# Kernel optimization log

Measured on AMD Instinct MI355X. Metric: run time of the kernel, lower is better.

Reference implementation:

```python
import jax, jax.numpy as jnp
import numpy as np
from jax.scipy.special import ndtr, ndtri, logsumexp

M_FREQ = 50
N_LAYERS = 5
MIXTURE = 5
MU = 4.0 * np.pi * 1e-7
LOG_2PI = float(np.log(2.0 * np.pi))
BATCH = 131072
SAMPL = 1


def setup_inputs() -> dict:
    key = jax.random.key(0)
    k1, k2, k3, k4 = jax.random.split(key, 4)
    x = jax.random.uniform(k1, (BATCH, N_LAYERS + 2 * M_FREQ), jnp.float32)
    s = jax.random.normal(k2, (BATCH, MIXTURE, 2 * N_LAYERS + 1), jnp.float32)
    u_cat = jax.random.uniform(k3, (SAMPL, BATCH), jnp.float32)
    u_trunc = jax.random.uniform(k4, (SAMPL, BATCH, N_LAYERS), jnp.float32)
    return {"x": x, "s": s, "u_cat": u_cat, "u_trunc": u_trunc}


def _elbo(x, s, u_cat, u_trunc):
    n = N_LAYERS
    B = x.shape[0]
    freqs = jnp.asarray(10.0 ** np.linspace(-2, 3, M_FREQ), jnp.float32)
    # --- mixture-density head ---
    sq = jnp.square(s[:, :, 2 * n])
    pro = sq / jnp.sum(sq, axis=1, keepdims=True)              # [B, M] (fun_part_uni)
    sig = jax.nn.softplus(s[:, :, n:2 * n])                    # [B, M, n]
    loc = 4.0 * jax.nn.sigmoid(s[:, :, :n])                    # [B, M, n]
    # --- sample q = Mixture(TruncatedNormal(loc, sig, 0.1, 3.9)) via inverse CDF ---
    cum = jnp.cumsum(pro, axis=1)                              # [B, M]
    comp = jnp.clip(jnp.sum(u_cat[:, :, None] > cum[None], axis=-1), 0, MIXTURE - 1)  # [S,B] int
    b_idx = jnp.arange(B)[None, :]
    loc_s = loc[b_idx, comp]                                   # [S, B, n]
    sig_s = sig[b_idx, comp]
    a = (0.1 - loc_s) / sig_s
    b = (3.9 - loc_s) / sig_s
    Fa, Fb = ndtr(a), ndtr(b)
    z = ndtri(Fa + u_trunc * (Fb - Fa))
    samples_q = jnp.clip(loc_s + sig_s * z, 0.1, 3.9)          # [S, B, n]
    # --- FP: recursive MT impedance forward model, vectorized over frequencies ---
    thick = x[:, :n]                                            # [B, n]
    res = 10.0 ** samples_q                                     # [S, B, n]
    w = (2.0 * np.pi) * freqs[:, None, None]                    # [m, 1, 1]
    ZR = jnp.sqrt(w * MU * res[:, :, n - 1] / 2.0)              # [m, S, B]
    ZC = ZR
    for j in range(n - 2, -1, -1):
        rj = res[:, :, j]                                       # [S, B]
        th = thick[:, j]                                        # [B]
        dj = jnp.sqrt(w * MU * (1.0 / rj) / 2.0)                # [m, S, B]
        wj = dj * rj                                            # wjR == wjC in source
        t = 2.0 * th * dj
        e = jnp.exp(-t)
        ejR = e * jnp.cos(t)   # cos(-t) == cos(t)
        ejC = -e * jnp.sin(t)
        den = jnp.square(wj + ZR) + jnp.square(wj + ZC)
        rjR = (2.0 * jnp.square(wj) - jnp.square(ZR) - jnp.square(ZC)) / den
        rjC = (2.0 * wj * ZR - 2.0 * wj * ZC) / den
        reR = rjR * ejR - rjC * ejC
        reC = rjR * ejC + rjC * ejR
        den2 = jnp.square(1.0 + reR) + jnp.square(reC)
        auxR = (1.0 - jnp.square(reR) - jnp.square(reC)) / den2
        auxC = -(2.0 * reC) / den2
        ZR, ZC = wj * auxR - wj * auxC, wj * auxC + wj * auxR
    absZ2 = jnp.square(ZR) + jnp.square(ZC)                     # [m, S, B]
    aRes = jnp.log10(absZ2 / (MU * w))
    phas = jnp.arctan2(ZC, ZR)
    S = samples_q.shape[0]
    formation = jnp.transpose(jnp.concatenate([aRes, phas], 0), (2, 1, 0)).reshape(S, B, 2 * M_FREQ)
    # --- ELBO terms ---
    obs = x[:, n:]                                              # [B, 2m]
    scale = jnp.abs(0.03 * formation)
    v = formation - obs[None]
    ll = -0.5 * jnp.square(v / scale) - jnp.log(scale) - 0.5 * LOG_2PI
    term_lik = -jnp.mean(ll)
    # q_ : same mixture with bounds (0, 4), log-prob at samples_q
    a_ = (0.0 - loc) / sig
    b_ = (4.0 - loc) / sig
    zc = (samples_q[:, :, None, :] - loc[None]) / sig[None]     # [S, B, M, n]
    comp_lp = jnp.sum(
        -0.5 * jnp.square(zc) - 0.5 * LOG_2PI - jnp.log(sig)[None]
        - jnp.log(ndtr(b_) - ndtr(a_))[None], axis=-1)          # [S, B, M]
    lq = logsumexp(jnp.log(pro)[None] + comp_lp, axis=-1)
    term_q = jnp.mean(lq)
    term_p = -jnp.log(jnp.float32(4.0))  # Uniform(0,4).log_prob, constant
    return term_lik + term_q - term_p


def reference(x, s, u_cat, u_trunc):
    return _elbo(x, s, u_cat, u_trunc)
```

## Files before the change

kernel.cpp:

```cpp
#include <hip/hip_runtime.h>
#include <math.h>

#define NL 5
#define KM 5
#define MF 50
#define BATCH_ 131072
#define XROW (NL + 2*MF)
#define SROW (KM*(2*NL+1))
#define LOG2PI_F 1.8378770664093453f

#define BPB 64
#define NB_FUSED (BATCH_/BPB)
#define NB_MONO  (BATCH_/256)

typedef float v2f __attribute__((ext_vector_type(2)));

__device__ __forceinline__ float rcpf_(float x)  { return __builtin_amdgcn_rcpf(x); }
__device__ __forceinline__ float sqrtf_(float x) { return __builtin_amdgcn_sqrtf(x); }
__device__ __forceinline__ float exp_(float x)   { return __expf(x); }
__device__ __forceinline__ float log_(float x)   { return __logf(x); }

__device__ __forceinline__ float ndtr_f(float x) {
    float z = fabsf(x) * 0.70710678f;
    float t = rcpf_(fmaf(0.3275911f, z, 1.0f));
    float poly = t*(0.254829592f + t*(-0.284496736f + t*(1.421413741f +
                 t*(-1.453152027f + t*1.061405429f))));
    float h = 0.5f * poly * exp_(-z*z);
    return x >= 0.0f ? 1.0f - h : h;
}

__device__ __forceinline__ float ndtri_f(float p) {
    float x = fmaf(2.0f, p, -1.0f);
    float w = -log_((1.0f - x) * (1.0f + x));
    float wc = w - 2.5f;
    float pc =            2.81022636e-08f;
    pc = fmaf(pc, wc,     3.43273939e-07f);
    pc = fmaf(pc, wc,    -3.5233877e-06f);
    pc = fmaf(pc, wc,    -4.39150654e-06f);
    pc = fmaf(pc, wc,     0.00021858087f);
    pc = fmaf(pc, wc,    -0.00125372503f);
    pc = fmaf(pc, wc,    -0.00417768164f);
    pc = fmaf(pc, wc,     0.246640727f);
    pc = fmaf(pc, wc,     1.50140941f);
    float wt = sqrtf_(w) - 3.0f;
    float pt =           -0.000200214257f;
    pt = fmaf(pt, wt,     0.000100950558f);
    pt = fmaf(pt, wt,     0.00134934322f);
    pt = fmaf(pt, wt,    -0.00367342844f);
    pt = fmaf(pt, wt,     0.00573950773f);
    pt = fmaf(pt, wt,    -0.0076224613f);
    pt = fmaf(pt, wt,     0.00943887047f);
    pt = fmaf(pt, wt,     1.00167406f);
    pt = fmaf(pt, wt,     2.83297682f);
    float r = (w < 5.0f) ? pc : pt;
    return 1.41421356f * r * x;
}

__device__ __forceinline__ float atan2_f(float y, float x) {
    float ax = fabsf(x), ay = fabsf(y);
    float mx = fmaxf(ax, ay), mn = fminf(ax, ay);
    float a = mn * rcpf_(mx);
    float s = a * a;
    float r =            -0.01172120f;
    r = fmaf(r, s,        0.05265332f);
    r = fmaf(r, s,       -0.11643287f);
    r = fmaf(r, s,        0.19354346f);
    r = fmaf(r, s,       -0.33262347f);
    r = fmaf(r, s,        0.99997726f);
    r = r * a;
    r = (ay > ax)   ? (1.5707964f - r) : r;
    r = (x < 0.0f)  ? (3.1415927f - r) : r;
    return (y < 0.0f) ? -r : r;
}

__device__ __forceinline__ float fwd_eval(int m, float sw, float oA, float oP,
                                          const float pr[9])
{
    float z0 = sw * pr[0];
    v2f Z = {z0, z0};
    #pragma unroll
    for (int j = NL-2; j >= 0; --j) {
        float wj = sw * pr[5+j];
        float t  = sw * pr[1+j];
        float t2 = t * t, t3 = t2 * t;
        float ejR = (1.0f - t) + t3 * fmaf(-0.16666667f, t, 0.33333334f);
        float ejC = fmaf(t3, -0.33333334f, t2) - t;
        v2f V = (v2f){wj, wj} - Z;
        v2f U = (v2f){wj, wj} + Z;
        v2f Vs = (v2f){-V.y, V.x};
        v2f W = ejR * V + ejC * Vs;
        v2f Nv = U - W;
        v2f D  = U + W;
        float invd = rcpf_(fmaf(D.x, D.x, D.y*D.y));
        float PR = fmaf(Nv.x, D.x,  Nv.y*D.y);
        float PC = fmaf(Nv.y, D.x, -Nv.x*D.y);
        float g  = wj * invd;
        Z = (v2f){g * (PR - PC), g * (PR + PC)};
    }
    float absZ2 = fmaf(Z.x, Z.x, Z.y*Z.y);
    float ex    = fmaf((float)m, 0.10204082f, -2.0f);
    float aRes  = fmaf(0.43429448f, log_(absZ2), 5.1026102f - ex);
    float ph    = atan2_f(Z.y, Z.x);
    float prod = aRes * ph;
    float ap   = fabsf(prod);
    float invp = rcpf_(ap);
    float vA = (aRes - oA) * (33.333332f * fabsf(ph)   * invp);
    float vP = (ph   - oP) * (33.333332f * fabsf(aRes) * invp);
    return fmaf(-0.5f, vA*vA, fmaf(-0.5f, vP*vP, 5.1752387f - log_(ap)));
}

__global__ void __launch_bounds__(256, 6) k_bnn(
    const float* __restrict__ x, const float* __restrict__ s,
    const float* __restrict__ u_cat, const float* __restrict__ u_trunc,
    float* __restrict__ p_ll, float* __restrict__ p_lq)
{
    __shared__ float lds_pr[BPB][12];
    __shared__ float lds_sw[MF];
    __shared__ float red0[4], red1[4];

    unsigned tid = threadIdx.x;
    unsigned bl = tid >> 2;
    unsigned i  = tid & 3;
    unsigned b  = blockIdx.x * BPB + bl;
    const float* srow = s + (size_t)b * SROW;

    if (tid < MF)
        lds_sw[tid] = 2.5066283f *
            exp_(1.1512925f * fmaf((float)tid, 0.10204082f, -2.0f));

    float pro[KM];
    float sqsum = 0.0f;
    #pragma unroll
    for (int k = 0; k < KM; ++k) {
        float v = srow[k*11 + 10];
        pro[k] = v * v;
        sqsum += pro[k];
    }
    float isq = rcpf_(sqsum);
    #pragma unroll
    for (int k = 0; k < KM; ++k) pro[k] *= isq;
    float u = u_cat[b];
    float cum = 0.0f; int cnt = 0;
    #pragma unroll
    for (int k = 0; k < KM; ++k) { cum += pro[k]; if (u > cum) ++cnt; }
    int comp = cnt < KM-1 ? cnt : KM-1;

    float cacc[KM];
    #pragma unroll
    for (int k = 0; k < KM; ++k) cacc[k] = 0.0f;

    #pragma unroll
    for (int r = 0; r < 2; ++r) {
        unsigned layer = i + 4u*r;
        bool active = (layer < NL);
        unsigned ll_ = active ? layer : i;
        float lc[KM], sg[KM];
        #pragma unroll
        for (int k = 0; k < KM; ++k) {
            lc[k] = 4.0f * rcpf_(1.0f + exp_(-srow[k*11 + ll_]));
            float sv = srow[k*11 + 5 + ll_];
            sg[k] = fmaxf(sv, 0.0f) + log_(1.0f + exp_(-fabsf(sv)));
        }
        float ls = lc[0], ss = sg[0];
        #pragma unroll
        for (int k = 1; k < KM; ++k) {
            bool sel = (k == comp);
            ls = sel ? lc[k] : ls;
            ss = sel ? sg[k] : ss;
        }
        float invss = rcpf_(ss);
        float a  = (0.1f - ls) * invss;
        float bb = (3.9f - ls) * invss;
        float Fa = ndtr_f(a), Fb = ndtr_f(bb);
        float p  = Fa + u_trunc[(size_t)b*NL + ll_] * (Fb - Fa);
        p = fminf(fmaxf(p, 0.0f), 1.0f);
        float z = ndtri_f(p);
        if (p <= 0.0f) z = -INFINITY;
        if (p >= 1.0f) z =  INFINITY;
        float smp = fminf(fmaxf(fmaf(ss, z, ls), 0.1f), 3.9f);

        #pragma unroll
        for (int k = 0; k < KM; ++k) {
            float invs = rcpf_(sg[k]);
            float zc = (smp - lc[k]) * invs;
            float a_ = (-lc[k]) * invs;
            float b_ = (4.0f - lc[k]) * invs;
            float Z  = ndtr_f(b_) - ndtr_f(a_);
            float v  = fmaf(-0.5f, zc*zc, -0.5f*LOG2PI_F) - log_(sg[k] * Z);
            cacc[k] += active ? v : 0.0f;
        }
        const float SQM = 7.9267442e-04f;
        const float HLN10 = 1.1512925f;
        float em  = exp_(-HLN10 * smp);
        float emi = SQM * rcpf_(em);
        if (r == 0) {
            float th = x[(size_t)b*XROW + i];
            lds_pr[bl][1+i] = 2.0f * th * SQM * em;
            lds_pr[bl][5+i] = emi;
        } else if (active) {
            lds_pr[bl][0] = emi;
        }
    }
    #pragma unroll
    for (int k = 0; k < KM; ++k) {
        cacc[k] += __shfl_xor(cacc[k], 1, 4);
        cacc[k] += __shfl_xor(cacc[k], 2, 4);
    }
    float mx = -INFINITY;
    float av[KM];
    #pragma unroll
    for (int k = 0; k < KM; ++k) { av[k] = log_(pro[k]) + cacc[k]; mx = fmaxf(mx, av[k]); }
    float se = 0.0f;
    #pragma unroll
    for (int k = 0; k < KM; ++k) se += exp_(av[k] - mx);
    float lqv = (i == 0) ? (mx + log_(se)) : 0.0f;

    __syncthreads();

    float pr[9];
    #pragma unroll
    for (int q = 0; q < 9; ++q) pr[q] = lds_pr[bl][q];
    const float* oArow = x + (size_t)b * XROW + NL;
    const float* oProw = oArow + MF;

    float ll = 0.0f;
    #pragma unroll
    for (int k = 0; k < 12; ++k) {
        int m = (int)i + 4*k;
        ll += fwd_eval(m, lds_sw[m], oArow[m], oProw[m], pr);
    }
    if (i < 2) {
        int m = (int)i + 48;
        ll += fwd_eval(m, lds_sw[m], oArow[m], oProw[m], pr);
    }

    #pragma unroll
    for (int off = 32; off > 0; off >>= 1) {
        ll  += __shfl_down(ll,  off, 64);
        lqv += __shfl_down(lqv, off, 64);
    }
    if ((tid & 63) == 0) {
        red0[tid >> 6] = ll;
        red1[tid >> 6] = lqv;
    }
    __syncthreads();
    if (tid == 0) {
        p_ll[blockIdx.x] = red0[0] + red0[1] + red0[2] + red0[3];
        p_lq[blockIdx.x] = red1[0] + red1[1] + red1[2] + red1[3];
    }
}

__global__ void __launch_bounds__(256) k_mono(
    const float* __restrict__ x, const float* __restrict__ s,
    const float* __restrict__ u_cat, const float* __restrict__ u_trunc,
    float* __restrict__ p_ll, float* __restrict__ p_lq)
{
    int b = blockIdx.x * 256 + threadIdx.x;
    const float* srow = s + (size_t)b * SROW;
    float loc[KM][NL], sig[KM][NL], pro[KM];
    float sqsum = 0.0f;
    #pragma unroll
    for (int k = 0; k < KM; ++k) { float v = srow[k*11+10]; pro[k] = v*v; sqsum += pro[k]; }
    float isq = rcpf_(sqsum);
    #pragma unroll
    for (int k = 0; k < KM; ++k) pro[k] *= isq;
    #pragma unroll
    for (int k = 0; k < KM; ++k)
        #pragma unroll
        for (int i = 0; i < NL; ++i) {
            loc[k][i] = 4.0f * rcpf_(1.0f + exp_(-srow[k*11+i]));
            float v = srow[k*11+5+i];
            sig[k][i] = fmaxf(v, 0.0f) + log_(1.0f + exp_(-fabsf(v)));
        }
    float u = u_cat[b];
    float cum = 0.0f; int cnt = 0;
    #pragma unroll
    for (int k = 0; k < KM; ++k) { cum += pro[k]; if (u > cum) ++cnt; }
    int comp = cnt < KM-1 ? cnt : KM-1;
    float ls[NL], ss[NL];
    #pragma unroll
    for (int i = 0; i < NL; ++i) { ls[i] = loc[0][i]; ss[i] = sig[0][i]; }
    #pragma unroll
    for (int k = 1; k < KM; ++k) {
        bool sel = (k == comp);
        #pragma unroll
        for (int i = 0; i < NL; ++i) {
            ls[i] = sel ? loc[k][i] : ls[i];
            ss[i] = sel ? sig[k][i] : ss[i];
        }
    }
    float smp[NL];
    #pragma unroll
    for (int i = 0; i < NL; ++i) {
        float invss = rcpf_(ss[i]);
        float a  = (0.1f - ls[i]) * invss;
        float bb = (3.9f - ls[i]) * invss;
        float Fa = ndtr_f(a), Fb = ndtr_f(bb);
        float p  = Fa + u_trunc[(size_t)b*NL + i] * (Fb - Fa);
        p = fminf(fmaxf(p, 0.0f), 1.0f);
        float z  = ndtri_f(p);
        if (p <= 0.0f) z = -INFINITY;
        if (p >= 1.0f) z =  INFINITY;
        smp[i] = fminf(fmaxf(fmaf(ss[i], z, ls[i]), 0.1f), 3.9f);
    }
    float vals[KM]; float mx = -INFINITY;
    #pragma unroll
    for (int k = 0; k < KM; ++k) {
        float av = log_(pro[k]);
        #pragma unroll
        for (int i = 0; i < NL; ++i) {
            float l = loc[k][i], sgv = sig[k][i];
            float invs = rcpf_(sgv);
            float zc = (smp[i] - l) * invs;
            float a_ = (-l) * invs;
            float b_ = (4.0f - l) * invs;
            float Z  = ndtr_f(b_) - ndtr_f(a_);
            av += fmaf(-0.5f, zc*zc, -0.5f*LOG2PI_F) - log_(sgv * Z);
        }
        vals[k] = av; mx = fmaxf(mx, av);
    }
    float se = 0.0f;
    #pragma unroll
    for (int k = 0; k < KM; ++k) se += exp_(vals[k] - mx);
    float lq = mx + log_(se);
    const float SQM = 7.9267442e-04f;
    const float HLN10 = 1.1512925f;
    float pr[9];
    pr[0] = SQM * exp_(HLN10 * smp[NL-1]);
    #pragma unroll
    for (int j = 0; j < NL-1; ++j) {
        float em = exp_(-HLN10 * smp[j]);
        float th = x[(size_t)b*XROW + j];
        pr[1+j] = 2.0f * th * SQM * em;
        pr[5+j] = SQM * rcpf_(em);
    }
    const float* xrow = x + (size_t)b * XROW;
    float ll = 0.0f;
    for (int m = 0; m < MF; ++m) {
        float sw = 2.5066283f * exp_(1.1512925f * fmaf((float)m, 0.10204082f, -2.0f));
        ll += fwd_eval(m, sw, xrow[NL + m], xrow[NL + MF + m], pr);
    }

    __shared__ float red0[4], red1[4];
    #pragma unroll
    for (int off = 32; off > 0; off >>= 1) {
        ll += __shfl_down(ll, off, 64);
        lq += __shfl_down(lq, off, 64);
    }
    if ((threadIdx.x & 63) == 0) { red0[threadIdx.x>>6] = ll; red1[threadIdx.x>>6] = lq; }
    __syncthreads();
    if (threadIdx.x == 0) {
        p_ll[blockIdx.x] = red0[0]+red0[1]+red0[2]+red0[3];
        p_lq[blockIdx.x] = red1[0]+red1[1]+red1[2]+red1[3];
    }
}

__global__ void __launch_bounds__(256) k_fin(
    const float* __restrict__ p_ll, const float* __restrict__ p_lq, int n,
    float* __restrict__ out)
{
    int tid = threadIdx.x;
    double a1 = 0.0, a0 = 0.0;
    for (int j = tid; j < n; j += 256) {
        a1 += (double)p_ll[j];
        a0 += (double)p_lq[j];
    }
    #pragma unroll
    for (int off = 32; off > 0; off >>= 1) {
        a0 += __shfl_down(a0, off, 64);
        a1 += __shfl_down(a1, off, 64);
    }
    __shared__ double r0[4], r1[4];
    if ((tid & 63) == 0) { r0[tid >> 6] = a0; r1[tid >> 6] = a1; }
    __syncthreads();
    if (tid == 0) {
        double A0 = r0[0]+r0[1]+r0[2]+r0[3];
        double A1 = r1[0]+r1[1]+r1[2]+r1[3];
        double term_lik = -A1 / ((double)BATCH_ * (double)(2*MF));
        double term_q   =  A0 / (double)BATCH_;
        out[0] = (float)(term_lik + term_q + 1.3862943611198906);
    }
}

extern "C" void kernel_launch(void* const* d_in, const int* in_sizes, int n_in,
                              void* d_out, int out_size, void* d_ws, size_t ws_size,
                              hipStream_t stream)
{
    (void)in_sizes; (void)n_in; (void)out_size;
    const float* x       = (const float*)d_in[0];
    const float* s       = (const float*)d_in[1];
    const float* u_cat   = (const float*)d_in[2];
    const float* u_trunc = (const float*)d_in[3];
    float* out = (float*)d_out;

    float* p_ll = (float*)d_ws;
    float* p_lq = p_ll + NB_FUSED;
    size_t needed = (size_t)2 * NB_FUSED * sizeof(float);

    if (ws_size >= needed) {
        k_bnn<<<NB_FUSED, 256, 0, stream>>>(x, s, u_cat, u_trunc, p_ll, p_lq);
        k_fin<<<1, 256, 0, stream>>>(p_ll, p_lq, NB_FUSED, out);
    } else {
        k_mono<<<NB_MONO, 256, 0, stream>>>(x, s, u_cat, u_trunc, p_ll, p_lq);
        k_fin<<<1, 256, 0, stream>>>(p_ll, p_lq, NB_MONO, out);
    }
}
```

Measured before the change: 145.4 us.

## Split fused kernel into 4-lane prologue and 8-lane frequency sweep per sample

The block now handles 32 samples instead of 64. Only the first 128 threads run the mixture/sampling prologue, still with 4 lanes per sample. All 256 threads then evaluate the forward model with 8 lanes per sample, 6 frequencies each, and the first 64 threads pick up the two leftover frequencies. The per-frequency sqrt(omega) factor is now updated by a multiply per step instead of being read from an LDS table. The aim is to spread the heavy frequency loop over more lanes and drop the 2-of-4 tail imbalance. In exchange, half the threads sit idle during the prologue, there are twice as many blocks, and the occupancy hint drops from 6 to 4.

```diff
diff --git a/kernel.cpp b/kernel.cpp
--- a/kernel.cpp
+++ b/kernel.cpp
@@ -9,7 +9,7 @@
 #define SROW (KM*(2*NL+1))
 #define LOG2PI_F 1.8378770664093453f
 
-#define BPB 64
+#define BPB 32
 #define NB_FUSED (BATCH_/BPB)
 #define NB_MONO  (BATCH_/256)
 
@@ -73,7 +73,7 @@
     return (y < 0.0f) ? -r : r;
 }
 
-__device__ __forceinline__ float fwd_eval(int m, float sw, float oA, float oP,
+__device__ __forceinline__ float fwd_eval(float ex, float sw, float oA, float oP,
                                           const float pr[9])
 {
     float z0 = sw * pr[0];
@@ -98,7 +98,6 @@
         Z = (v2f){g * (PR - PC), g * (PR + PC)};
     }
     float absZ2 = fmaf(Z.x, Z.x, Z.y*Z.y);
-    float ex    = fmaf((float)m, 0.10204082f, -2.0f);
     float aRes  = fmaf(0.43429448f, log_(absZ2), 5.1026102f - ex);
     float ph    = atan2_f(Z.y, Z.x);
     float prod = aRes * ph;
@@ -109,129 +108,142 @@
     return fmaf(-0.5f, vA*vA, fmaf(-0.5f, vP*vP, 5.1752387f - log_(ap)));
 }
 
-__global__ void __launch_bounds__(256, 6) k_bnn(
+__global__ void __launch_bounds__(256, 4) k_bnn(
     const float* __restrict__ x, const float* __restrict__ s,
     const float* __restrict__ u_cat, const float* __restrict__ u_trunc,
     float* __restrict__ p_ll, float* __restrict__ p_lq)
 {
     __shared__ float lds_pr[BPB][12];
-    __shared__ float lds_sw[MF];
     __shared__ float red0[4], red1[4];
 
     unsigned tid = threadIdx.x;
-    unsigned bl = tid >> 2;
-    unsigned i  = tid & 3;
-    unsigned b  = blockIdx.x * BPB + bl;
-    const float* srow = s + (size_t)b * SROW;
-
-    if (tid < MF)
-        lds_sw[tid] = 2.5066283f *
-            exp_(1.1512925f * fmaf((float)tid, 0.10204082f, -2.0f));
-
-    float pro[KM];
-    float sqsum = 0.0f;
-    #pragma unroll
-    for (int k = 0; k < KM; ++k) {
-        float v = srow[k*11 + 10];
-        pro[k] = v * v;
-        sqsum += pro[k];
-    }
-    float isq = rcpf_(sqsum);
-    #pragma unroll
-    for (int k = 0; k < KM; ++k) pro[k] *= isq;
-    float u = u_cat[b];
-    float cum = 0.0f; int cnt = 0;
-    #pragma unroll
-    for (int k = 0; k < KM; ++k) { cum += pro[k]; if (u > cum) ++cnt; }
-    int comp = cnt < KM-1 ? cnt : KM-1;
-
-    float cacc[KM];
-    #pragma unroll
-    for (int k = 0; k < KM; ++k) cacc[k] = 0.0f;
-
-    #pragma unroll
-    for (int r = 0; r < 2; ++r) {
-        unsigned layer = i + 4u*r;
-        bool active = (layer < NL);
-        unsigned ll_ = active ? layer : i;
-        float lc[KM], sg[KM];
+    float lqv = 0.0f;
+
+    if (tid < 128) {
+        unsigned bl = tid >> 2;
+        unsigned i  = tid & 3;
+        unsigned b  = blockIdx.x * BPB + bl;
+        const float* srow = s + (size_t)b * SROW;
+
+        float pro[KM];
+        float sqsum = 0.0f;
         #pragma unroll
         for (int k = 0; k < KM; ++k) {
-            lc[k] = 4.0f * rcpf_(1.0f + exp_(-srow[k*11 + ll_]));
-            float sv = srow[k*11 + 5 + ll_];
-            sg[k] = fmaxf(sv, 0.0f) + log_(1.0f + exp_(-fabsf(sv)));
-        }
-        float ls = lc[0], ss = sg[0];
-        #pragma unroll
-        for (int k = 1; k < KM; ++k) {
-            bool sel = (k == comp);
-            ls = sel ? lc[k] : ls;
-            ss = sel ? sg[k] : ss;
-        }
-        float invss = rcpf_(ss);
-        float a  = (0.1f - ls) * invss;
-        float bb = (3.9f - ls) * invss;
-        float Fa = ndtr_f(a), Fb = ndtr_f(bb);
-        float p  = Fa + u_trunc[(size_t)b*NL + ll_] * (Fb - Fa);
-        p = fminf(fmaxf(p, 0.0f), 1.0f);
-        float z = ndtri_f(p);
-        if (p <= 0.0f) z = -INFINITY;
-        if (p >= 1.0f) z =  INFINITY;
-        float smp = fminf(fmaxf(fmaf(ss, z, ls), 0.1f), 3.9f);
-
+            float v = srow[k*11 + 10];
+            pro[k] = v * v;
+            sqsum += pro[k];
+        }
+        float isq = rcpf_(sqsum);
+        #pragma unroll
+        for (int k = 0; k < KM; ++k) pro[k] *= isq;
+        float u = u_cat[b];
+        float cum = 0.0f; int cnt = 0;
+        #pragma unroll
+        for (int k = 0; k < KM; ++k) { cum += pro[k]; if (u > cum) ++cnt; }
+        int comp = cnt < KM-1 ? cnt : KM-1;
+
+        float cacc[KM];
+        #pragma unroll
+        for (int k = 0; k < KM; ++k) cacc[k] = 0.0f;
+
+        #pragma unroll
+        for (int r = 0; r < 2; ++r) {
+            unsigned layer = i + 4u*r;
+            bool active = (layer < NL);
+            unsigned ll_ = active ? layer : i;
+            float lc[KM], sg[KM];
+            #pragma unroll
+            for (int k = 0; k < KM; ++k) {
+                lc[k] = 4.0f * rcpf_(1.0f + exp_(-srow[k*11 + ll_]));
+                float sv = srow[k*11 + 5 + ll_];
+                sg[k] = fmaxf(sv, 0.0f) + log_(1.0f + exp_(-fabsf(sv)));
+            }
+            float ls = lc[0], ss = sg[0];
+            #pragma unroll
+            for (int k = 1; k < KM; ++k) {
+                bool sel = (k == comp);
+                ls = sel ? lc[k] : ls;
+                ss = sel ? sg[k] : ss;
+            }
+            float invss = rcpf_(ss);
+            float a  = (0.1f - ls) * invss;
+            float bb = (3.9f - ls) * invss;
+            float Fa = ndtr_f(a), Fb = ndtr_f(bb);
+            float p  = Fa + u_trunc[(size_t)b*NL + ll_] * (Fb - Fa);
+            p = fminf(fmaxf(p, 0.0f), 1.0f);
+            float z = ndtri_f(p);
+            if (p <= 0.0f) z = -INFINITY;
+            if (p >= 1.0f) z =  INFINITY;
+            float smp = fminf(fmaxf(fmaf(ss, z, ls), 0.1f), 3.9f);
+
+            #pragma unroll
+            for (int k = 0; k < KM; ++k) {
+                float invs = rcpf_(sg[k]);
+                float zc = (smp - lc[k]) * invs;
+                float a_ = (-lc[k]) * invs;
+                float b_ = (4.0f - lc[k]) * invs;
+                float Z  = ndtr_f(b_) - ndtr_f(a_);
+                float v  = fmaf(-0.5f, zc*zc, -0.5f*LOG2PI_F) - log_(sg[k] * Z);
+                cacc[k] += active ? v : 0.0f;
+            }
+            const float SQM = 7.9267442e-04f;
+            const float HLN10 = 1.1512925f;
+            float em  = exp_(-HLN10 * smp);
+            float emi = SQM * rcpf_(em);
+            if (r == 0) {
+                float th = x[(size_t)b*XROW + i];
+                lds_pr[bl][1+i] = 2.0f * th * SQM * em;
+                lds_pr[bl][5+i] = emi;
+            } else if (active) {
+                lds_pr[bl][0] = emi;
+            }
+        }
         #pragma unroll
         for (int k = 0; k < KM; ++k) {
-            float invs = rcpf_(sg[k]);
-            float zc = (smp - lc[k]) * invs;
-            float a_ = (-lc[k]) * invs;
-            float b_ = (4.0f - lc[k]) * invs;
-            float Z  = ndtr_f(b_) - ndtr_f(a_);
-            float v  = fmaf(-0.5f, zc*zc, -0.5f*LOG2PI_F) - log_(sg[k] * Z);
-            cacc[k] += active ? v : 0.0f;
-        }
-        const float SQM = 7.9267442e-04f;
-        const float HLN10 = 1.1512925f;
-        float em  = exp_(-HLN10 * smp);
-        float emi = SQM * rcpf_(em);
-        if (r == 0) {
-            float th = x[(size_t)b*XROW + i];
-            lds_pr[bl][1+i] = 2.0f * th * SQM * em;
-            lds_pr[bl][5+i] = emi;
-        } else if (active) {
-            lds_pr[bl][0] = emi;
-        }
-    }
-    #pragma unroll
-    for (int k = 0; k < KM; ++k) {
-        cacc[k] += __shfl_xor(cacc[k], 1, 4);
-        cacc[k] += __shfl_xor(cacc[k], 2, 4);
-    }
-    float mx = -INFINITY;
-    float av[KM];
-    #pragma unroll
-    for (int k = 0; k < KM; ++k) { av[k] = log_(pro[k]) + cacc[k]; mx = fmaxf(mx, av[k]); }
-    float se = 0.0f;
-    #pragma unroll
-    for (int k = 0; k < KM; ++k) se += exp_(av[k] - mx);
-    float lqv = (i == 0) ? (mx + log_(se)) : 0.0f;
-
+            cacc[k] += __shfl_xor(cacc[k], 1, 4);
+            cacc[k] += __shfl_xor(cacc[k], 2, 4);
+        }
+        float mx = -INFINITY;
+        float av[KM];
+        #pragma unroll
+        for (int k = 0; k < KM; ++k) { av[k] = log_(pro[k]) + cacc[k]; mx = fmaxf(mx, av[k]); }
+        float se = 0.0f;
+        #pragma unroll
+        for (int k = 0; k < KM; ++k) se += exp_(av[k] - mx);
+        if (i == 0) lqv = mx + log_(se);
+    }
     __syncthreads();
 
+    unsigned bl8 = tid >> 3;
+    unsigned i8  = tid & 7;
+    unsigned b8  = blockIdx.x * BPB + bl8;
     float pr[9];
     #pragma unroll
-    for (int q = 0; q < 9; ++q) pr[q] = lds_pr[bl][q];
-    const float* oArow = x + (size_t)b * XROW + NL;
+    for (int q = 0; q < 9; ++q) pr[q] = lds_pr[bl8][q];
+    const float* oArow = x + (size_t)b8 * XROW + NL;
     const float* oProw = oArow + MF;
 
+    float ex = fmaf((float)i8, 0.10204082f, -2.0f);
+    float sw = 2.5066283f * exp_(1.1512925f * ex);
     float ll = 0.0f;
     #pragma unroll
-    for (int k = 0; k < 12; ++k) {
-        int m = (int)i + 4*k;
-        ll += fwd_eval(m, lds_sw[m], oArow[m], oProw[m], pr);
-    }
-    if (i < 2) {
-        int m = (int)i + 48;
-        ll += fwd_eval(m, lds_sw[m], oArow[m], oProw[m], pr);
+    for (int k = 0; k < 6; ++k) {
+        int m = (int)i8 + 8*k;
+        ll += fwd_eval(ex, sw, oArow[m], oProw[m], pr);
+        ex += 0.81632653f;
+        sw *= 2.5595522f;
+    }
+    if (tid < 64) {
+        unsigned blt = tid >> 1;
+        int mt = 48 + (int)(tid & 1);
+        unsigned bt = blockIdx.x * BPB + blt;
+        float prt[9];
+        #pragma unroll
+        for (int q = 0; q < 9; ++q) prt[q] = lds_pr[blt][q];
+        float ext = fmaf((float)mt, 0.10204082f, -2.0f);
+        float swt = 2.5066283f * exp_(1.1512925f * ext);
+        const float* xr = x + (size_t)bt * XROW;
+        ll += fwd_eval(ext, swt, xr[NL + mt], xr[NL + MF + mt], prt);
     }
 
     #pragma unroll
@@ -337,8 +349,9 @@
     const float* xrow = x + (size_t)b * XROW;
     float ll = 0.0f;
     for (int m = 0; m < MF; ++m) {
-        float sw = 2.5066283f * exp_(1.1512925f * fmaf((float)m, 0.10204082f, -2.0f));
-        ll += fwd_eval(m, sw, xrow[NL + m], xrow[NL + MF + m], pr);
+        float ex = fmaf((float)m, 0.10204082f, -2.0f);
+        float sw = 2.5066283f * exp_(1.1512925f * ex);
+        ll += fwd_eval(ex, sw, xrow[NL + m], xrow[NL + MF + m], pr);
     }
 
     __shared__ float red0[4], red1[4];
```

New measurement: 147.3 us. About the same (+1.3%).

## Use two threads per batch row with contiguous frequency halves

Applied to the files above, without the earlier changes.

Each batch row is now handled by 2 threads instead of 4. Each thread computes 3 layers of the mixture head and then 25 consecutive frequencies, so the block shrinks to 128 threads. The per-frequency constants (sqrt-omega and the log offset) are advanced by a multiply and a subtract in each iteration, replacing the LDS table, and observation loads become contiguous per thread. This cuts redundant per-row head work and shuffles. The cost is less parallelism per row, and accumulating the frequency factor step by step can drift in float precision.

```diff
diff --git a/kernel.cpp b/kernel.cpp
--- a/kernel.cpp
+++ b/kernel.cpp
@@ -10,6 +10,7 @@
 #define LOG2PI_F 1.8378770664093453f
 
 #define BPB 64
+#define TPB 128
 #define NB_FUSED (BATCH_/BPB)
 #define NB_MONO  (BATCH_/256)
 
@@ -73,7 +74,7 @@
     return (y < 0.0f) ? -r : r;
 }
 
-__device__ __forceinline__ float fwd_eval(int m, float sw, float oA, float oP,
+__device__ __forceinline__ float fwd_eval(float c5, float sw, float oA, float oP,
                                           const float pr[9])
 {
     float z0 = sw * pr[0];
@@ -98,8 +99,7 @@
         Z = (v2f){g * (PR - PC), g * (PR + PC)};
     }
     float absZ2 = fmaf(Z.x, Z.x, Z.y*Z.y);
-    float ex    = fmaf((float)m, 0.10204082f, -2.0f);
-    float aRes  = fmaf(0.43429448f, log_(absZ2), 5.1026102f - ex);
+    float aRes  = fmaf(0.43429448f, log_(absZ2), c5);
     float ph    = atan2_f(Z.y, Z.x);
     float prod = aRes * ph;
     float ap   = fabsf(prod);
@@ -109,24 +109,20 @@
     return fmaf(-0.5f, vA*vA, fmaf(-0.5f, vP*vP, 5.1752387f - log_(ap)));
 }
 
-__global__ void __launch_bounds__(256, 6) k_bnn(
+__global__ void __launch_bounds__(TPB, 8) k_bnn(
     const float* __restrict__ x, const float* __restrict__ s,
     const float* __restrict__ u_cat, const float* __restrict__ u_trunc,
     float* __restrict__ p_ll, float* __restrict__ p_lq)
 {
-    __shared__ float lds_pr[BPB][12];
-    __shared__ float lds_sw[MF];
-    __shared__ float red0[4], red1[4];
+    __shared__ float lds_pr[BPB][13];
+    __shared__ float red0[2], red1[2];
 
     unsigned tid = threadIdx.x;
-    unsigned bl = tid >> 2;
-    unsigned i  = tid & 3;
+    unsigned bl = tid >> 1;
+    unsigned i  = tid & 1;
     unsigned b  = blockIdx.x * BPB + bl;
     const float* srow = s + (size_t)b * SROW;
-
-    if (tid < MF)
-        lds_sw[tid] = 2.5066283f *
-            exp_(1.1512925f * fmaf((float)tid, 0.10204082f, -2.0f));
+    float lqv = 0.0f;
 
     float pro[KM];
     float sqsum = 0.0f;
@@ -150,8 +146,8 @@
     for (int k = 0; k < KM; ++k) cacc[k] = 0.0f;
 
     #pragma unroll
-    for (int r = 0; r < 2; ++r) {
-        unsigned layer = i + 4u*r;
+    for (int r = 0; r < 3; ++r) {
+        unsigned layer = i + 2u*r;
         bool active = (layer < NL);
         unsigned ll_ = active ? layer : i;
         float lc[KM], sg[KM];
@@ -193,45 +189,44 @@
         const float HLN10 = 1.1512925f;
         float em  = exp_(-HLN10 * smp);
         float emi = SQM * rcpf_(em);
-        if (r == 0) {
-            float th = x[(size_t)b*XROW + i];
-            lds_pr[bl][1+i] = 2.0f * th * SQM * em;
-            lds_pr[bl][5+i] = emi;
+        if (r < 2) {
+            float th = x[(size_t)b*XROW + layer];
+            lds_pr[bl][1+layer] = 2.0f * th * SQM * em;
+            lds_pr[bl][5+layer] = emi;
         } else if (active) {
             lds_pr[bl][0] = emi;
         }
     }
     #pragma unroll
-    for (int k = 0; k < KM; ++k) {
-        cacc[k] += __shfl_xor(cacc[k], 1, 4);
-        cacc[k] += __shfl_xor(cacc[k], 2, 4);
-    }
-    float mx = -INFINITY;
-    float av[KM];
-    #pragma unroll
-    for (int k = 0; k < KM; ++k) { av[k] = log_(pro[k]) + cacc[k]; mx = fmaxf(mx, av[k]); }
-    float se = 0.0f;
-    #pragma unroll
-    for (int k = 0; k < KM; ++k) se += exp_(av[k] - mx);
-    float lqv = (i == 0) ? (mx + log_(se)) : 0.0f;
-
+    for (int k = 0; k < KM; ++k)
+        cacc[k] += __shfl_xor(cacc[k], 1, 2);
+    {
+        float mx = -INFINITY;
+        float av[KM];
+        #pragma unroll
+        for (int k = 0; k < KM; ++k) { av[k] = log_(pro[k]) + cacc[k]; mx = fmaxf(mx, av[k]); }
+        float se = 0.0f;
+        #pragma unroll
+        for (int k = 0; k < KM; ++k) se += exp_(av[k] - mx);
+        if (i == 0) lqv = mx + log_(se);
+    }
     __syncthreads();
 
     float pr[9];
     #pragma unroll
     for (int q = 0; q < 9; ++q) pr[q] = lds_pr[bl][q];
-    const float* oArow = x + (size_t)b * XROW + NL;
+    const float* oArow = x + (size_t)b * XROW + NL + 25u*i;
     const float* oProw = oArow + MF;
 
+    float ex = fmaf((float)(25u*i), 0.10204082f, -2.0f);
+    float c5 = 5.1026102f - ex;
+    float sw = 2.5066283f * exp_(1.1512925f * ex);
     float ll = 0.0f;
     #pragma unroll
-    for (int k = 0; k < 12; ++k) {
-        int m = (int)i + 4*k;
-        ll += fwd_eval(m, lds_sw[m], oArow[m], oProw[m], pr);
-    }
-    if (i < 2) {
-        int m = (int)i + 48;
-        ll += fwd_eval(m, lds_sw[m], oArow[m], oProw[m], pr);
+    for (int k = 0; k < 25; ++k) {
+        ll += fwd_eval(c5, sw, oArow[k], oProw[k], pr);
+        c5 -= 0.10204082f;
+        sw *= 1.1246574f;
     }
 
     #pragma unroll
@@ -245,8 +240,8 @@
     }
     __syncthreads();
     if (tid == 0) {
-        p_ll[blockIdx.x] = red0[0] + red0[1] + red0[2] + red0[3];
-        p_lq[blockIdx.x] = red1[0] + red1[1] + red1[2] + red1[3];
+        p_ll[blockIdx.x] = red0[0] + red0[1];
+        p_lq[blockIdx.x] = red1[0] + red1[1];
     }
 }
 
@@ -337,8 +332,9 @@
     const float* xrow = x + (size_t)b * XROW;
     float ll = 0.0f;
     for (int m = 0; m < MF; ++m) {
-        float sw = 2.5066283f * exp_(1.1512925f * fmaf((float)m, 0.10204082f, -2.0f));
-        ll += fwd_eval(m, sw, xrow[NL + m], xrow[NL + MF + m], pr);
+        float ex = fmaf((float)m, 0.10204082f, -2.0f);
+        float sw = 2.5066283f * exp_(1.1512925f * ex);
+        ll += fwd_eval(5.1026102f - ex, sw, xrow[NL + m], xrow[NL + MF + m], pr);
     }
 
     __shared__ float red0[4], red1[4];
@@ -398,7 +394,7 @@
     size_t needed = (size_t)2 * NB_FUSED * sizeof(float);
 
     if (ws_size >= needed) {
-        k_bnn<<<NB_FUSED, 256, 0, stream>>>(x, s, u_cat, u_trunc, p_ll, p_lq);
+        k_bnn<<<NB_FUSED, TPB, 0, stream>>>(x, s, u_cat, u_trunc, p_ll, p_lq);
         k_fin<<<1, 256, 0, stream>>>(p_ll, p_lq, NB_FUSED, out);
     } else {
         k_mono<<<NB_MONO, 256, 0, stream>>>(x, s, u_cat, u_trunc, p_ll, p_lq);
```

New measurement: 152.2 us. 1.05x slower.
